# Performance work log

Hardware: AMD Instinct MI355X
Metric: run time of the kernel (lower is better)

## Reference

```python
import jax, jax.numpy as jnp
import numpy as np

SOFTMAX_TEMP = 0.01
WINDOW_SIZE = 2


def setup_inputs() -> dict:
    key = jax.random.key(0)
    k1, k2, k3, k4 = jax.random.split(key, 4)
    bsz, C, N, H, W = 8, 248, 512, 256, 256
    return {
        "keypoint_scores": jax.random.uniform(k1, (bsz, 1, N), dtype=jnp.float32),
        "keypoint_desc": jax.random.normal(k2, (bsz, C, N), dtype=jnp.float32),
        "scores_dense": jax.random.uniform(k3, (bsz, 1, H, W), dtype=jnp.float32),
        "desc_dense": jax.random.normal(k4, (bsz, C, H, W), dtype=jnp.float32),
    }


def reference(keypoint_scores, keypoint_desc, scores_dense, desc_dense):
    w = WINDOW_SIZE
    bsz, C, N = keypoint_desc.shape
    B = bsz // w  # batch_size (number of windows)
    H, Wd = desc_dense.shape[2], desc_dense.shape[3]
    HW = H * Wd

    # dense pixel coords: meshgrid 'ij' -> v over H, u over W; coords = stack(u, v)
    v_coord, u_coord = jnp.meshgrid(jnp.arange(H, dtype=jnp.float32),
                                    jnp.arange(Wd, dtype=jnp.float32), indexing="ij")
    coords = jnp.stack((u_coord.reshape(HW), v_coord.reshape(HW)), axis=1)  # [HW, 2]

    # source frame of each window: every window_size-th item, L2-normalized over C
    src = desc_dense[::w].reshape(B, C, HW)  # [B, C, HW]
    src = src / jnp.linalg.norm(src, axis=1, keepdims=True).clip(1e-12)

    # target frames: indices i*w + 1 .. i*w + w-1 for each window i
    tgt_ids = (jnp.arange(B)[:, None] * w + jnp.arange(1, w)[None, :]).reshape(-1)  # [B*(w-1)]
    tgt = keypoint_desc[tgt_ids].reshape(B, w - 1, C, N)  # [B, w-1, C, N]

    # similarity of each keypoint vs dense src grid; temperature softmax over grid
    match = jnp.einsum("bwcn,bch->bwnh", tgt, src)  # [B, w-1, N, HW]
    soft = jax.nn.softmax(match / SOFTMAX_TEMP, axis=-1)

    # expected 2D coordinate per keypoint
    pseudo = jnp.einsum("bwnh,hd->bwnd", soft, coords)  # [B, w-1, N, 2]
    pseudo_coords = pseudo.reshape(B * (w - 1), N, 2)

    return pseudo_coords, keypoint_scores[tgt_ids], tgt_ids
```

## Files before the change

kernel.cpp:

```cpp
#include <hip/hip_runtime.h>
#include <stdint.h>
#include <stddef.h>

#define C_DIM 248
#define N_KP 512
#define HW_PIX 65536
#define NWIN 4
#define NTILE 32
#define NQ 4
#define GROUPS32 2048
#define SCALE_LOG2 144.2695041f

typedef __attribute__((ext_vector_type(8))) _Float16 f16x8;
typedef __attribute__((ext_vector_type(4))) float f32x4;

__device__ __forceinline__ float fexp2(float x) {
    return __builtin_amdgcn_exp2f(x);
}

__global__ __launch_bounds__(256) void k_prep(const float* __restrict__ kd,
                                              f16x8* __restrict__ Bws) {
    int g = blockIdx.x * 256 + threadIdx.x;
    int c15 = g & 15;
    int l4 = (g >> 4) & 3;
    int kk = (g >> 6) & 7;
    int t  = (g >> 9) & 31;
    int b  = g >> 14;
    int col = t * 16 + c15;
    const float* base = kd + (size_t)(2 * b + 1) * C_DIM * N_KP;
    f16x8 hv;
    #pragma unroll
    for (int j = 0; j < 8; ++j) {
        int c = kk * 32 + l4 * 8 + j;
        float v = (c < C_DIM) ? base[(size_t)c * N_KP + col] : 0.0f;
        hv[j] = (_Float16)v;
    }
    Bws[(size_t)(b * 32 + t) * 512 + kk * 64 + l4 * 16 + c15] = hv;
}

__global__ __launch_bounds__(512, 1) void k_main(const float* __restrict__ dd,
                                                 const f16x8* __restrict__ Bws,
                                                 float4* __restrict__ partials) {
    int b = blockIdx.x >> 8;
    int grp = blockIdx.x & 255;
    int tid = threadIdx.x;
    int lane = tid & 63;
    int wave = tid >> 6;
    int l15 = lane & 15;
    int l4 = lane >> 4;
    int pw = grp * 256 + wave * 32;
    int g32 = grp * 8 + wave;

    __shared__ __align__(16) short Bbuf[2][32768];

    const f16x8* Bwin = Bws + (size_t)b * 32 * 512;
    #define STAGE(slot_, q_)                                                          \
        {                                                                             \
            const f16x8* src_ = Bwin + (size_t)(q_) * 4096;                           \
            _Pragma("unroll")                                                         \
            for (int i_ = 0; i_ < 8; ++i_) {                                          \
                __builtin_amdgcn_global_load_lds(                                     \
                    (const __attribute__((address_space(1))) void*)                   \
                        (src_ + i_ * 512 + wave * 64 + lane),                         \
                    (__attribute__((address_space(3))) void*)                         \
                        ((char*)&Bbuf[slot_][0] + (i_ * 512 + wave * 64) * 16),       \
                    16, 0, 0);                                                        \
            }                                                                         \
        }

    STAGE(0, 0)

    const float* srcp = dd + (size_t)(2 * b) * C_DIM * HW_PIX;
    f16x8 aH[2][8];
    float ss[2] = {0.f, 0.f};
    #pragma unroll
    for (int s = 0; s < 2; ++s) {
        #pragma unroll
        for (int kk = 0; kk < 8; ++kk) {
            #pragma unroll
            for (int j = 0; j < 8; ++j) {
                int c = kk * 32 + l4 * 8 + j;
                float v = (c < C_DIM) ? srcp[(size_t)c * HW_PIX + pw + s * 16 + l15] : 0.0f;
                ss[s] = fmaf(v, v, ss[s]);
                aH[s][kk][j] = (_Float16)v;
            }
        }
        ss[s] += __shfl_xor(ss[s], 16);
        ss[s] += __shfl_xor(ss[s], 32);
    }
    float srow[2][4];
    #pragma unroll
    for (int s = 0; s < 2; ++s) {
        #pragma unroll
        for (int r = 0; r < 4; ++r) {
            float ssr = __shfl(ss[s], l4 * 4 + r);
            srow[s][r] = SCALE_LOG2 / fmaxf(sqrtf(ssr), 1e-12f);
        }
    }
    float ubase = (float)((pw & 255) + l4 * 4);

    asm volatile("s_waitcnt vmcnt(0)" ::: "memory");
    __builtin_amdgcn_s_barrier();

    for (int q = 0; q < NQ; ++q) {
        if (q + 1 < NQ) STAGE((q + 1) & 1, q + 1)

        const short* qbase = &Bbuf[q & 1][0];
        #pragma unroll 2
        for (int tt = 0; tt < 8; ++tt) {
            int t = q * 8 + tt;
            const f16x8* Bt = (const f16x8*)(qbase + tt * 4096);
            f32x4 acc[2][2];
            #pragma unroll
            for (int s = 0; s < 2; ++s)
                #pragma unroll
                for (int qq = 0; qq < 2; ++qq) acc[s][qq] = (f32x4){0.f, 0.f, 0.f, 0.f};

            #pragma unroll
            for (int kp = 0; kp < 4; ++kp) {
                f16x8 b0 = Bt[(2 * kp) * 64 + lane];
                f16x8 b1 = Bt[(2 * kp + 1) * 64 + lane];
                acc[0][0] = __builtin_amdgcn_mfma_f32_16x16x32_f16(aH[0][2 * kp], b0, acc[0][0], 0, 0, 0);
                acc[1][0] = __builtin_amdgcn_mfma_f32_16x16x32_f16(aH[1][2 * kp], b0, acc[1][0], 0, 0, 0);
                acc[0][1] = __builtin_amdgcn_mfma_f32_16x16x32_f16(aH[0][2 * kp + 1], b1, acc[0][1], 0, 0, 0);
                acc[1][1] = __builtin_amdgcn_mfma_f32_16x16x32_f16(aH[1][2 * kp + 1], b1, acc[1][1], 0, 0, 0);
            }

            float lg[2][4];
            float m = -3.0e38f;
            #pragma unroll
            for (int s = 0; s < 2; ++s)
                #pragma unroll
                for (int r = 0; r < 4; ++r) {
                    lg[s][r] = (acc[s][0][r] + acc[s][1][r]) * srow[s][r];
                    m = fmaxf(m, lg[s][r]);
                }
            float d = 0.f, sx = 0.f;
            #pragma unroll
            for (int s = 0; s < 2; ++s)
                #pragma unroll
                for (int r = 0; r < 4; ++r) {
                    float e = fexp2(lg[s][r] - m);
                    d += e;
                    sx = fmaf(e, ubase + (float)(s * 16 + r), sx);
                }
            #pragma unroll
            for (int off = 16; off <= 32; off <<= 1) {
                float m2 = __shfl_xor(m, off);
                float d2 = __shfl_xor(d, off);
                float sx2 = __shfl_xor(sx, off);
                float Mn = fmaxf(m, m2);
                float c1 = fexp2(m - Mn);
                float c2 = fexp2(m2 - Mn);
                d  = d * c1 + d2 * c2;
                sx = sx * c1 + sx2 * c2;
                m = Mn;
            }
            if (lane < 16) {
                float4 p; p.x = m; p.y = d; p.z = sx; p.w = 0.f;
                partials[((size_t)b * GROUPS32 + g32) * 512 + t * 16 + l15] = p;
            }
        }

        if (q + 1 < NQ) {
            asm volatile("s_waitcnt vmcnt(8)" ::: "memory");
            __builtin_amdgcn_s_barrier();
        }
    }
    #undef STAGE
}

__global__ __launch_bounds__(256) void k_reduce(const float4* __restrict__ partials,
                                                const float* __restrict__ ksc,
                                                float* __restrict__ out) {
    int b = blockIdx.x >> 6;
    int kc = blockIdx.x & 63;
    int tid = threadIdx.x;
    int kpo = tid & 7;
    int gs = tid >> 3;
    int kp = kc * 8 + kpo;

    float M = -1e30f, D = 0.f, SX = 0.f, SY = 0.f;
    for (int g = gs; g < GROUPS32; g += 32) {
        float4 p = partials[((size_t)b * GROUPS32 + g) * 512 + kp];
        float vg = (float)(g >> 3);
        float Mn = fmaxf(M, p.x);
        float c1 = fexp2(M - Mn);
        float c2 = fexp2(p.x - Mn);
        D  = D  * c1 + p.y * c2;
        SX = SX * c1 + p.z * c2;
        SY = SY * c1 + vg * p.y * c2;
        M = Mn;
    }
    __shared__ float4 red[32][8];
    float4 me; me.x = M; me.y = D; me.z = SX; me.w = SY;
    red[gs][kpo] = me;
    __syncthreads();
    if (gs == 0) {
        #pragma unroll
        for (int w = 1; w < 32; ++w) {
            float4 p = red[w][kpo];
            float Mn = fmaxf(M, p.x);
            float c1 = fexp2(M - Mn);
            float c2 = fexp2(p.x - Mn);
            D  = D  * c1 + p.y * c2;
            SX = SX * c1 + p.z * c2;
            SY = SY * c1 + p.w * c2;
            M = Mn;
        }
        int flat = b * 512 + kp;
        out[flat * 2 + 0] = SX / D;
        out[flat * 2 + 1] = SY / D;
        out[4096 + flat] = ksc[(size_t)(2 * b + 1) * N_KP + kp];
    }
    if (blockIdx.x == 0 && tid < 4) out[6144 + tid] = (float)(2 * tid + 1);
}

extern "C" void kernel_launch(void* const* d_in, const int* in_sizes, int n_in,
                              void* d_out, int out_size, void* d_ws, size_t ws_size,
                              hipStream_t stream) {
    const float* kp_scores  = (const float*)d_in[0];
    const float* kp_desc    = (const float*)d_in[1];
    const float* desc_dense = (const float*)d_in[3];
    float* out = (float*)d_out;

    f16x8* Bws = (f16x8*)d_ws;
    float4* partials = (float4*)((char*)d_ws + (size_t)NWIN * 32 * 512 * 16);

    k_prep<<<256, 256, 0, stream>>>(kp_desc, Bws);
    k_main<<<NWIN * 256, 512, 0, stream>>>(desc_dense, Bws, partials);
    k_reduce<<<NWIN * 64, 256, 0, stream>>>(partials, kp_scores, out);
}
```

Measured before the change: 183.9 us.

## Process two pixel tiles per block, prefetching second A tile during first pass

Each block now handles 512 pixels in two sequential passes over the keypoint descriptors, which halves the grid. The dense-descriptor loads for the second tile are issued during the last quarter of the first pass, so global latency overlaps with MFMA work. The B staging pipeline wraps around so the second pass can start without a cold load. s_setprio is also raised around the MFMA section. In exchange, register pressure rises from holding a second A fragment, and the grid (512 blocks) may leave compute units less evenly loaded.

```diff
diff --git a/kernel.cpp b/kernel.cpp
--- a/kernel.cpp
+++ b/kernel.cpp
@@ -41,15 +41,15 @@
 __global__ __launch_bounds__(512, 1) void k_main(const float* __restrict__ dd,
                                                  const f16x8* __restrict__ Bws,
                                                  float4* __restrict__ partials) {
-    int b = blockIdx.x >> 8;
-    int grp = blockIdx.x & 255;
+    int b = blockIdx.x >> 7;
+    int grp = blockIdx.x & 127;
     int tid = threadIdx.x;
     int lane = tid & 63;
     int wave = tid >> 6;
     int l15 = lane & 15;
     int l4 = lane >> 4;
-    int pw = grp * 256 + wave * 32;
-    int g32 = grp * 8 + wave;
+    int pw0 = grp * 512 + wave * 32;
+    int pw1 = pw0 + 256;
 
     __shared__ __align__(16) short Bbuf[2][32768];
 
@@ -71,8 +71,9 @@
     STAGE(0, 0)
 
     const float* srcp = dd + (size_t)(2 * b) * C_DIM * HW_PIX;
-    f16x8 aH[2][8];
-    float ss[2] = {0.f, 0.f};
+
+    f16x8 aH0[2][8];
+    float ss0[2] = {0.f, 0.f};
     #pragma unroll
     for (int s = 0; s < 2; ++s) {
         #pragma unroll
@@ -80,86 +81,137 @@
             #pragma unroll
             for (int j = 0; j < 8; ++j) {
                 int c = kk * 32 + l4 * 8 + j;
-                float v = (c < C_DIM) ? srcp[(size_t)c * HW_PIX + pw + s * 16 + l15] : 0.0f;
-                ss[s] = fmaf(v, v, ss[s]);
-                aH[s][kk][j] = (_Float16)v;
+                float v = (c < C_DIM) ? srcp[(size_t)c * HW_PIX + pw0 + s * 16 + l15] : 0.0f;
+                ss0[s] = fmaf(v, v, ss0[s]);
+                aH0[s][kk][j] = (_Float16)v;
             }
         }
-        ss[s] += __shfl_xor(ss[s], 16);
-        ss[s] += __shfl_xor(ss[s], 32);
-    }
-    float srow[2][4];
-    #pragma unroll
-    for (int s = 0; s < 2; ++s) {
+        ss0[s] += __shfl_xor(ss0[s], 16);
+        ss0[s] += __shfl_xor(ss0[s], 32);
+    }
+    float srow0[2][4];
+    #pragma unroll
+    for (int s = 0; s < 2; ++s)
         #pragma unroll
         for (int r = 0; r < 4; ++r) {
-            float ssr = __shfl(ss[s], l4 * 4 + r);
-            srow[s][r] = SCALE_LOG2 / fmaxf(sqrtf(ssr), 1e-12f);
-        }
-    }
-    float ubase = (float)((pw & 255) + l4 * 4);
+            float ssr = __shfl(ss0[s], l4 * 4 + r);
+            srow0[s][r] = SCALE_LOG2 / fmaxf(sqrtf(ssr), 1e-12f);
+        }
+    float ubase = (float)((wave << 5) + l4 * 4);
+
+    f16x8 aH1[2][8];
+    float ss1[2] = {0.f, 0.f};
+    float srow1[2][4];
+
+    #define DO_TILE(AH_, SROW_, G32_, T_, QB_)                                        \
+        {                                                                             \
+            const f16x8* Bt_ = (const f16x8*)((QB_));                                 \
+            f32x4 acc[2][2];                                                          \
+            _Pragma("unroll")                                                         \
+            for (int s = 0; s < 2; ++s)                                               \
+                _Pragma("unroll")                                                     \
+                for (int qq = 0; qq < 2; ++qq) acc[s][qq] = (f32x4){0.f,0.f,0.f,0.f}; \
+            __builtin_amdgcn_s_setprio(1);                                            \
+            _Pragma("unroll")                                                         \
+            for (int kp = 0; kp < 4; ++kp) {                                          \
+                f16x8 b0 = Bt_[(2 * kp) * 64 + lane];                                 \
+                f16x8 b1 = Bt_[(2 * kp + 1) * 64 + lane];                             \
+                acc[0][0] = __builtin_amdgcn_mfma_f32_16x16x32_f16(AH_[0][2*kp],   b0, acc[0][0], 0, 0, 0); \
+                acc[1][0] = __builtin_amdgcn_mfma_f32_16x16x32_f16(AH_[1][2*kp],   b0, acc[1][0], 0, 0, 0); \
+                acc[0][1] = __builtin_amdgcn_mfma_f32_16x16x32_f16(AH_[0][2*kp+1], b1, acc[0][1], 0, 0, 0); \
+                acc[1][1] = __builtin_amdgcn_mfma_f32_16x16x32_f16(AH_[1][2*kp+1], b1, acc[1][1], 0, 0, 0); \
+            }                                                                         \
+            __builtin_amdgcn_s_setprio(0);                                            \
+            float lg[2][4];                                                           \
+            float m = -3.0e38f;                                                       \
+            _Pragma("unroll")                                                         \
+            for (int s = 0; s < 2; ++s)                                               \
+                _Pragma("unroll")                                                     \
+                for (int r = 0; r < 4; ++r) {                                         \
+                    lg[s][r] = (acc[s][0][r] + acc[s][1][r]) * SROW_[s][r];           \
+                    m = fmaxf(m, lg[s][r]);                                           \
+                }                                                                     \
+            float d = 0.f, sx = 0.f;                                                  \
+            _Pragma("unroll")                                                         \
+            for (int s = 0; s < 2; ++s)                                               \
+                _Pragma("unroll")                                                     \
+                for (int r = 0; r < 4; ++r) {                                         \
+                    float e = fexp2(lg[s][r] - m);                                    \
+                    d += e;                                                           \
+                    sx = fmaf(e, ubase + (float)(s * 16 + r), sx);                    \
+                }                                                                     \
+            _Pragma("unroll")                                                         \
+            for (int off = 16; off <= 32; off <<= 1) {                                \
+                float m2 = __shfl_xor(m, off);                                        \
+                float d2 = __shfl_xor(d, off);                                        \
+                float sx2 = __shfl_xor(sx, off);                                      \
+                float Mn = fmaxf(m, m2);                                              \
+                float c1 = fexp2(m - Mn);                                             \
+                float c2 = fexp2(m2 - Mn);                                            \
+                d  = d * c1 + d2 * c2;                                                \
+                sx = sx * c1 + sx2 * c2;                                              \
+                m = Mn;                                                               \
+            }                                                                         \
+            if (lane < 16) {                                                          \
+                float4 p; p.x = m; p.y = d; p.z = sx; p.w = 0.f;                      \
+                partials[((size_t)b * GROUPS32 + (G32_)) * 512 + (T_) * 16 + l15] = p;\
+            }                                                                         \
+        }
 
     asm volatile("s_waitcnt vmcnt(0)" ::: "memory");
     __builtin_amdgcn_s_barrier();
 
+    int g32a = grp * 16 + wave;
     for (int q = 0; q < NQ; ++q) {
-        if (q + 1 < NQ) STAGE((q + 1) & 1, q + 1)
+        STAGE((q + 1) & 1, (q + 1) & 3)
+
+        if (q == 3) {
+            #pragma unroll
+            for (int s = 0; s < 2; ++s) {
+                #pragma unroll
+                for (int kk = 0; kk < 8; ++kk) {
+                    #pragma unroll
+                    for (int j = 0; j < 8; ++j) {
+                        int c = kk * 32 + l4 * 8 + j;
+                        float v = (c < C_DIM) ? srcp[(size_t)c * HW_PIX + pw1 + s * 16 + l15] : 0.0f;
+                        ss1[s] = fmaf(v, v, ss1[s]);
+                        aH1[s][kk][j] = (_Float16)v;
+                    }
+                }
+            }
+        }
 
         const short* qbase = &Bbuf[q & 1][0];
         #pragma unroll 2
         for (int tt = 0; tt < 8; ++tt) {
-            int t = q * 8 + tt;
-            const f16x8* Bt = (const f16x8*)(qbase + tt * 4096);
-            f32x4 acc[2][2];
-            #pragma unroll
-            for (int s = 0; s < 2; ++s)
-                #pragma unroll
-                for (int qq = 0; qq < 2; ++qq) acc[s][qq] = (f32x4){0.f, 0.f, 0.f, 0.f};
-
-            #pragma unroll
-            for (int kp = 0; kp < 4; ++kp) {
-                f16x8 b0 = Bt[(2 * kp) * 64 + lane];
-                f16x8 b1 = Bt[(2 * kp + 1) * 64 + lane];
-                acc[0][0] = __builtin_amdgcn_mfma_f32_16x16x32_f16(aH[0][2 * kp], b0, acc[0][0], 0, 0, 0);
-                acc[1][0] = __builtin_amdgcn_mfma_f32_16x16x32_f16(aH[1][2 * kp], b0, acc[1][0], 0, 0, 0);
-                acc[0][1] = __builtin_amdgcn_mfma_f32_16x16x32_f16(aH[0][2 * kp + 1], b1, acc[0][1], 0, 0, 0);
-                acc[1][1] = __builtin_amdgcn_mfma_f32_16x16x32_f16(aH[1][2 * kp + 1], b1, acc[1][1], 0, 0, 0);
-            }
-
-            float lg[2][4];
-            float m = -3.0e38f;
-            #pragma unroll
-            for (int s = 0; s < 2; ++s)
-                #pragma unroll
-                for (int r = 0; r < 4; ++r) {
-                    lg[s][r] = (acc[s][0][r] + acc[s][1][r]) * srow[s][r];
-                    m = fmaxf(m, lg[s][r]);
-                }
-            float d = 0.f, sx = 0.f;
-            #pragma unroll
-            for (int s = 0; s < 2; ++s)
-                #pragma unroll
-                for (int r = 0; r < 4; ++r) {
-                    float e = fexp2(lg[s][r] - m);
-                    d += e;
-                    sx = fmaf(e, ubase + (float)(s * 16 + r), sx);
-                }
-            #pragma unroll
-            for (int off = 16; off <= 32; off <<= 1) {
-                float m2 = __shfl_xor(m, off);
-                float d2 = __shfl_xor(d, off);
-                float sx2 = __shfl_xor(sx, off);
-                float Mn = fmaxf(m, m2);
-                float c1 = fexp2(m - Mn);
-                float c2 = fexp2(m2 - Mn);
-                d  = d * c1 + d2 * c2;
-                sx = sx * c1 + sx2 * c2;
-                m = Mn;
-            }
-            if (lane < 16) {
-                float4 p; p.x = m; p.y = d; p.z = sx; p.w = 0.f;
-                partials[((size_t)b * GROUPS32 + g32) * 512 + t * 16 + l15] = p;
-            }
+            DO_TILE(aH0, srow0, g32a, q * 8 + tt, qbase + tt * 4096)
+        }
+
+        asm volatile("s_waitcnt vmcnt(8)" ::: "memory");
+        __builtin_amdgcn_s_barrier();
+    }
+
+    #pragma unroll
+    for (int s = 0; s < 2; ++s) {
+        ss1[s] += __shfl_xor(ss1[s], 16);
+        ss1[s] += __shfl_xor(ss1[s], 32);
+    }
+    #pragma unroll
+    for (int s = 0; s < 2; ++s)
+        #pragma unroll
+        for (int r = 0; r < 4; ++r) {
+            float ssr = __shfl(ss1[s], l4 * 4 + r);
+            srow1[s][r] = SCALE_LOG2 / fmaxf(sqrtf(ssr), 1e-12f);
+        }
+
+    int g32b = grp * 16 + 8 + wave;
+    for (int q = 0; q < NQ; ++q) {
+        if (q + 1 < NQ) STAGE((q + 1) & 1, q + 1)
+
+        const short* qbase = &Bbuf[q & 1][0];
+        #pragma unroll 2
+        for (int tt = 0; tt < 8; ++tt) {
+            DO_TILE(aH1, srow1, g32b, q * 8 + tt, qbase + tt * 4096)
         }
 
         if (q + 1 < NQ) {
@@ -167,6 +219,7 @@
             __builtin_amdgcn_s_barrier();
         }
     }
+    #undef DO_TILE
     #undef STAGE
 }
 
@@ -228,6 +281,6 @@
     float4* partials = (float4*)((char*)d_ws + (size_t)NWIN * 32 * 512 * 16);
 
     k_prep<<<256, 256, 0, stream>>>(kp_desc, Bws);
-    k_main<<<NWIN * 256, 512, 0, stream>>>(desc_dense, Bws, partials);
+    k_main<<<NWIN * 128, 512, 0, stream>>>(desc_dense, Bws, partials);
     k_reduce<<<NWIN * 64, 256, 0, stream>>>(partials, kp_scores, out);
 }
```

Result: slower. 327.3 us (+78.0%).
